# Kernel tuning notes

Hardware: AMD Instinct MI355X
Metric: run time of the kernel (lower is better)

Reference implementation:

```python
import jax, jax.numpy as jnp
import numpy as np

GAMMA = 0.99
LMBDA = 0.95


def setup_inputs() -> dict:
    key = jax.random.key(0)
    k1, k2, k3, k4 = jax.random.split(key, 4)
    B, T = 4096, 2048
    return {
        "reward": jax.random.normal(k1, (B, T), dtype=jnp.float32),
        "terminated": jax.random.randint(k2, (B, T), 0, 2, dtype=jnp.int32),
        "value": jax.random.normal(k3, (B, T), dtype=jnp.float32),
        "next_value": jax.random.normal(k4, (B, T), dtype=jnp.float32),
    }


def _gae(reward, not_done, value, next_value):
    # All inputs [B, T]. Backward-time scan over T with carry gae [B].
    # delta_t = r_t + gamma * V(s_{t+1}) * nd_t - V(s_t)
    # A_t = delta_t + gamma * lmbda * nd_t * A_{t+1}
    xs = (reward.T, not_done.T, value.T, next_value.T)  # each [T, B]

    def step(gae, x):
        r, nd, v, nv = x
        delta = r + GAMMA * nv * nd - v
        gae = delta + GAMMA * LMBDA * nd * gae
        return gae, gae

    init = jnp.zeros(reward.shape[0], dtype=reward.dtype)
    _, adv_t = jax.lax.scan(step, init, xs, reverse=True)  # [T, B]
    advantages = adv_t.T  # [B, T]
    returns = advantages + value
    return advantages, returns


def reference(reward, terminated, value, next_value):
    not_done = 1.0 - terminated.astype(reward.dtype)
    return _gae(reward, not_done, value, next_value)
```

## Files before the change

### kernel.cpp

```cpp
#include <hip/hip_runtime.h>
#include <stdint.h>


constexpr float GAMMA = 0.99f;
constexpr float LMBDA = 0.95f;
constexpr int   T     = 2048;
constexpr int   TPB   = 512;
constexpr int   E     = T / TPB;
constexpr int   NW    = TPB / 64;
constexpr int   RPB   = 4;

typedef float f4 __attribute__((ext_vector_type(4)));

typedef __attribute__((address_space(1))) void  as1_void;
typedef __attribute__((address_space(3))) void  as3_void;

__device__ __forceinline__ void stage16(const void* g, void* s) {
    __builtin_amdgcn_global_load_lds((as1_void*)g, (as3_void*)s, 16, 0, 0);
}

__global__ __launch_bounds__(TPB, 8) void gae_kernel(
    const float* __restrict__ reward,
    const int*   __restrict__ term,
    const float* __restrict__ value,
    const float* __restrict__ next_value,
    float* __restrict__ adv_out,
    float* __restrict__ ret_out)
{
    const int j    = threadIdx.x;
    const int wave = j >> 6;
    const int lane = j & 63;

    __shared__ float sRew[T];
    __shared__ int   sTrm[T];
    __shared__ float sVal[T];
    __shared__ float sNxt[T];
    __shared__ float sAf[2][NW];
    __shared__ float sBf[2][NW];

    const size_t tbase = (size_t)blockIdx.x * (RPB * T) + (size_t)j * E;
    const int    wofs  = wave << 8;

    stage16(reward     + tbase, sRew + wofs);
    stage16(term       + tbase, sTrm + wofs);
    stage16(value      + tbase, sVal + wofs);
    stage16(next_value + tbase, sNxt + wofs);
    asm volatile("s_waitcnt vmcnt(0)" ::: "memory");

    #pragma unroll 1
    for (int k = 0; k < RPB; ++k) {
        asm volatile("s_waitcnt vmcnt(2)" ::: "memory");

        const f4   rv = *(const f4*  )(sRew + j * E);
        const int4 tv = *(const int4*)(sTrm + j * E);
        const f4   vv = *(const f4*  )(sVal + j * E);
        const f4   nx = *(const f4*  )(sNxt + j * E);

        asm volatile("s_waitcnt lgkmcnt(0)" ::: "memory");
        if (k + 1 < RPB) {
            const size_t nb = tbase + (size_t)(k + 1) * T;
            stage16(reward     + nb, sRew + wofs);
            stage16(term       + nb, sTrm + wofs);
            stage16(value      + nb, sVal + wofs);
            stage16(next_value + nb, sNxt + wofs);
        }
        asm volatile("" ::: "memory");

        const float r [E] = {rv[0], rv[1], rv[2], rv[3]};
        const float nd[E] = {1.f - (float)tv.x, 1.f - (float)tv.y,
                             1.f - (float)tv.z, 1.f - (float)tv.w};
        const float v [E] = {vv[0], vv[1], vv[2], vv[3]};
        const float nxv[E]= {nx[0], nx[1], nx[2], nx[3]};

        float loc[E], P[E];
        {
            float g = 0.f, p = 1.f;
            #pragma unroll
            for (int t = E - 1; t >= 0; --t) {
                const float c     = (GAMMA * LMBDA) * nd[t];
                const float delta = fmaf(GAMMA * nxv[t], nd[t], r[t]) - v[t];
                g = fmaf(c, g, delta);
                p *= c;
                loc[t] = g;
                P[t]   = p;
            }
        }

        float A = loc[0], Bc = P[0];
        #pragma unroll
        for (int off = 1; off < 64; off <<= 1) {
            const float a2 = __shfl_down(A,  off, 64);
            const float b2 = __shfl_down(Bc, off, 64);
            if (lane + off < 64) {
                A  = fmaf(Bc, a2, A);
                Bc *= b2;
            }
        }

        const int pb = k & 1;
        if (lane == 0) { sAf[pb][wave] = A; sBf[pb][wave] = Bc; }

        float eA = __shfl_down(A,  1, 64);
        float eB = __shfl_down(Bc, 1, 64);
        if (lane == 63) { eA = 0.f; eB = 1.f; }

        asm volatile("s_waitcnt lgkmcnt(0)" ::: "memory");
        __builtin_amdgcn_s_barrier();
        asm volatile("" ::: "memory");

        float wcarry = 0.f;
        #pragma unroll
        for (int w = NW - 1; w > 0; --w) {
            if (w > wave) wcarry = fmaf(sBf[pb][w], wcarry, sAf[pb][w]);
        }

        const float gin = fmaf(eB, wcarry, eA);

        f4 a4, q4;
        #pragma unroll
        for (int t = 0; t < E; ++t) {
            const float a = fmaf(P[t], gin, loc[t]);
            a4[t] = a;
            q4[t] = a + v[t];
        }
        const size_t gb = tbase + (size_t)k * T;
        __builtin_nontemporal_store(a4, (f4*)(adv_out + gb));
        __builtin_nontemporal_store(q4, (f4*)(ret_out + gb));
    }
}

extern "C" void kernel_launch(void* const* d_in, const int* in_sizes, int n_in,
                              void* d_out, int out_size, void* d_ws, size_t ws_size,
                              hipStream_t stream) {
    const float* reward     = (const float*)d_in[0];
    const int*   term       = (const int*  )d_in[1];
    const float* value      = (const float*)d_in[2];
    const float* next_value = (const float*)d_in[3];

    const int BT = in_sizes[0];
    const int B  = BT / T;

    float* adv = (float*)d_out;
    float* ret = adv + BT;

    gae_kernel<<<B / RPB, TPB, 0, stream>>>(reward, term, value, next_value, adv, ret);
}
```

Baseline: 178.3 us.

## Replace LDS-staged global_load_lds with register-prefetched direct global loads

Removes the LDS staging buffers and global_load_lds path. Each thread now loads its four 16-byte vectors straight into registers and prefetches the next row's data while computing the current row. The row loop is fully unrolled and launch bounds drop from 8 to 6 waves per SIMD. This avoids the LDS round trip and the waitcnt fences, at the cost of more VGPRs and possibly lower occupancy.

```diff
diff --git a/kernel.cpp b/kernel.cpp
--- a/kernel.cpp
+++ b/kernel.cpp
@@ -1,9 +1,9 @@
 #include <hip/hip_runtime.h>
-#include <stdint.h>
 
 
 constexpr float GAMMA = 0.99f;
 constexpr float LMBDA = 0.95f;
+constexpr float GL    = GAMMA * LMBDA;
 constexpr int   T     = 2048;
 constexpr int   TPB   = 512;
 constexpr int   E     = T / TPB;
@@ -12,14 +12,7 @@
 
 typedef float f4 __attribute__((ext_vector_type(4)));
 
-typedef __attribute__((address_space(1))) void  as1_void;
-typedef __attribute__((address_space(3))) void  as3_void;
-
-__device__ __forceinline__ void stage16(const void* g, void* s) {
-    __builtin_amdgcn_global_load_lds((as1_void*)g, (as3_void*)s, 16, 0, 0);
-}
-
-__global__ __launch_bounds__(TPB, 8) void gae_kernel(
+__global__ __launch_bounds__(TPB, 6) void gae_kernel(
     const float* __restrict__ reward,
     const int*   __restrict__ term,
     const float* __restrict__ value,
@@ -31,62 +24,51 @@
     const int wave = j >> 6;
     const int lane = j & 63;
 
-    __shared__ float sRew[T];
-    __shared__ int   sTrm[T];
-    __shared__ float sVal[T];
-    __shared__ float sNxt[T];
     __shared__ float sAf[2][NW];
     __shared__ float sBf[2][NW];
 
     const size_t tbase = (size_t)blockIdx.x * (RPB * T) + (size_t)j * E;
-    const int    wofs  = wave << 8;
 
-    stage16(reward     + tbase, sRew + wofs);
-    stage16(term       + tbase, sTrm + wofs);
-    stage16(value      + tbase, sVal + wofs);
-    stage16(next_value + tbase, sNxt + wofs);
-    asm volatile("s_waitcnt vmcnt(0)" ::: "memory");
+    f4   rv = *(const f4*  )(reward     + tbase);
+    int4 tv = *(const int4*)(term       + tbase);
+    f4   vv = *(const f4*  )(value      + tbase);
+    f4   nx = *(const f4*  )(next_value + tbase);
 
-    #pragma unroll 1
+    #pragma unroll
     for (int k = 0; k < RPB; ++k) {
-        asm volatile("s_waitcnt vmcnt(2)" ::: "memory");
-
-        const f4   rv = *(const f4*  )(sRew + j * E);
-        const int4 tv = *(const int4*)(sTrm + j * E);
-        const f4   vv = *(const f4*  )(sVal + j * E);
-        const f4   nx = *(const f4*  )(sNxt + j * E);
-
-        asm volatile("s_waitcnt lgkmcnt(0)" ::: "memory");
+        f4 rv2, vv2, nx2; int4 tv2;
         if (k + 1 < RPB) {
             const size_t nb = tbase + (size_t)(k + 1) * T;
-            stage16(reward     + nb, sRew + wofs);
-            stage16(term       + nb, sTrm + wofs);
-            stage16(value      + nb, sVal + wofs);
-            stage16(next_value + nb, sNxt + wofs);
+            rv2 = *(const f4*  )(reward     + nb);
+            tv2 = *(const int4*)(term       + nb);
+            vv2 = *(const f4*  )(value      + nb);
+            nx2 = *(const f4*  )(next_value + nb);
         }
-        asm volatile("" ::: "memory");
 
-        const float r [E] = {rv[0], rv[1], rv[2], rv[3]};
-        const float nd[E] = {1.f - (float)tv.x, 1.f - (float)tv.y,
-                             1.f - (float)tv.z, 1.f - (float)tv.w};
-        const float v [E] = {vv[0], vv[1], vv[2], vv[3]};
-        const float nxv[E]= {nx[0], nx[1], nx[2], nx[3]};
+        float c[E], d[E], v[E];
+        {
+            const int ti[E] = {tv.x, tv.y, tv.z, tv.w};
+            #pragma unroll
+            for (int u = 0; u < E; ++u) {
+                const float nd = 1.f - (float)ti[u];
+                v[u] = vv[u];
+                c[u] = GL * nd;
+                d[u] = fmaf(GAMMA * nx[u], nd, rv[u]) - vv[u];
+            }
+        }
 
-        float loc[E], P[E];
         {
             float g = 0.f, p = 1.f;
             #pragma unroll
             for (int t = E - 1; t >= 0; --t) {
-                const float c     = (GAMMA * LMBDA) * nd[t];
-                const float delta = fmaf(GAMMA * nxv[t], nd[t], r[t]) - v[t];
-                g = fmaf(c, g, delta);
-                p *= c;
-                loc[t] = g;
-                P[t]   = p;
+                g = fmaf(c[t], g, d[t]);
+                p *= c[t];
+                d[t] = g;
+                c[t] = p;
             }
         }
 
-        float A = loc[0], Bc = P[0];
+        float A = d[0], Bc = c[0];
         #pragma unroll
         for (int off = 1; off < 64; off <<= 1) {
             const float a2 = __shfl_down(A,  off, 64);
@@ -119,13 +101,15 @@
         f4 a4, q4;
         #pragma unroll
         for (int t = 0; t < E; ++t) {
-            const float a = fmaf(P[t], gin, loc[t]);
+            const float a = fmaf(c[t], gin, d[t]);
             a4[t] = a;
             q4[t] = a + v[t];
         }
         const size_t gb = tbase + (size_t)k * T;
         __builtin_nontemporal_store(a4, (f4*)(adv_out + gb));
         __builtin_nontemporal_store(q4, (f4*)(ret_out + gb));
+
+        if (k + 1 < RPB) { rv = rv2; tv = tv2; vv = vv2; nx = nx2; }
     }
 }
 
```

Measured after the change: 179.3 us. About the same (+0.6%).
